# Optimization experiments

Hardware: AMD Instinct MI355X
Metric: run time of the kernel (lower is better)

The kernel has to match this reference:

```python
import jax, jax.numpy as jnp
import numpy as np


def _layer_norm(x, g, b, eps=1e-5):
    mu = jnp.mean(x, axis=-1, keepdims=True)
    var = jnp.mean((x - mu) ** 2, axis=-1, keepdims=True)
    return (x - mu) * jax.lax.rsqrt(var + eps) * g + b


def setup_inputs() -> dict:
    key = jax.random.key(0)
    ks = jax.random.split(key, 12)
    L, D, HD, F, V, MAXLEN, B, S = 4, 1024, 64, 4096, 32000, 2048, 2, 1024
    s = 0.02
    return {
        "x": jax.random.randint(ks[0], (B, S), 0, V, dtype=jnp.int32),
        "tok_emb": jax.random.normal(ks[1], (V, D), jnp.float32) * s,
        "pos_emb": jax.random.normal(ks[2], (MAXLEN, D), jnp.float32) * s,
        "wq": jax.random.normal(ks[3], (L, HD, HD), jnp.float32) * s,
        "wk": jax.random.normal(ks[4], (L, HD, HD), jnp.float32) * s,
        "wv": jax.random.normal(ks[5], (L, HD, HD), jnp.float32) * s,
        "wo": jax.random.normal(ks[6], (L, D, D), jnp.float32) * s,
        "bo": jnp.zeros((L, D), jnp.float32),
        "ln1_g": jnp.ones((L, D), jnp.float32),
        "ln1_b": jnp.zeros((L, D), jnp.float32),
        "ln2_g": jnp.ones((L, D), jnp.float32),
        "ln2_b": jnp.zeros((L, D), jnp.float32),
        "w1": jax.random.normal(ks[7], (L, F, D), jnp.float32) * s,
        "b1": jnp.zeros((L, F), jnp.float32),
        "w2": jax.random.normal(ks[8], (L, D, F), jnp.float32) * s,
        "b2": jnp.zeros((L, D), jnp.float32),
        "out_w": jax.random.normal(ks[9], (V, D), jnp.float32) * s,
        "out_b": jnp.zeros((V,), jnp.float32),
    }


def reference(x, tok_emb, pos_emb, wq, wk, wv, wo, bo, ln1_g, ln1_b, ln2_g, ln2_b, w1, b1, w2, b2, out_w, out_b):
    B, S = x.shape
    D = tok_emb.shape[1]
    HD = wq.shape[-1]
    H = D // HD
    inv_scale = 1.0 / jnp.sqrt(jnp.asarray(D, jnp.float32))  # note: embed_size, not head_dim

    h = tok_emb[x] + pos_emb[:S][None]  # [B,S,D]; dropout is identity in eval

    def block(h, p):
        pwq, pwk, pwv, pwo, pbo, g1, be1, g2, be2, pw1, pb1, pw2, pb2 = p
        xh = h.reshape(B, S, H, HD)
        # per-head Linear with shared [HD,HD] weight: y = x @ W.T
        q = jnp.einsum('bshd,ed->bshe', xh, pwq)
        k = jnp.einsum('bshd,ed->bshe', xh, pwk)
        v = jnp.einsum('bshd,ed->bshe', xh, pwv)
        energy = jnp.einsum('bqhd,bkhd->bhqk', q, k)  # full [B,H,S,S] scores
        attn = jax.nn.softmax(energy * inv_scale, axis=-1)
        o = jnp.einsum('bhqk,bkhd->bqhd', attn, v).reshape(B, S, D)
        o = o @ pwo.T + pbo
        x1 = _layer_norm(o + h, g1, be1)
        ff = jax.nn.gelu(x1 @ pw1.T + pb1, approximate=False) @ pw2.T + pb2
        return _layer_norm(ff + x1, g2, be2), None

    h, _ = jax.lax.scan(block, h, (wq, wk, wv, wo, bo, ln1_g, ln1_b, ln2_g, ln2_b, w1, b1, w2, b2))
    return h @ out_w.T + out_b  # [B,S,V] logits
```

## Files before the change

kernel.cpp:

```cpp
#include <hip/hip_runtime.h>
#include <math.h>

typedef float f32x4 __attribute__((ext_vector_type(4)));
typedef unsigned short u16x8 __attribute__((ext_vector_type(8)));
typedef unsigned short u16x4 __attribute__((ext_vector_type(4)));
typedef __bf16 bf16x8 __attribute__((ext_vector_type(8)));
typedef unsigned int u32;

#define DEV static __device__ __forceinline__

DEV unsigned short f2bf(float f) {
  __bf16 h = (__bf16)f;
  return __builtin_bit_cast(unsigned short, h);
}
DEV float bf2f(unsigned short s) { return __uint_as_float(((unsigned)s) << 16); }
DEV bf16x8 asbf(u16x8 v) { return __builtin_bit_cast(bf16x8, v); }

DEV void gload16(const void* g, void* l) {
  __builtin_amdgcn_global_load_lds((const __attribute__((address_space(1))) u32*)g,
                                   (__attribute__((address_space(3))) u32*)l, 16, 0, 0);
}

__global__ void cvt_kernel(const float* __restrict__ in, unsigned short* __restrict__ out, int n8) {
  for (int i = blockIdx.x * 256 + threadIdx.x; i < n8; i += gridDim.x * 256) {
    const float* s = in + (size_t)i * 8;
    f32x4 a = *(const f32x4*)s, b = *(const f32x4*)(s + 4);
    u16x8 o;
    for (int j = 0; j < 4; ++j) { o[j] = f2bf(a[j]); o[j + 4] = f2bf(b[j]); }
    *(u16x8*)(out + (size_t)i * 8) = o;
  }
}

__global__ void cvt2_kernel(const float* __restrict__ s0, unsigned short* __restrict__ d0, int na,
                            const float* __restrict__ s1, unsigned short* __restrict__ d1, int nb) {
  int total = na + nb;
  for (int i = blockIdx.x * 256 + threadIdx.x; i < total; i += gridDim.x * 256) {
    const float* s; unsigned short* d; int k;
    if (i < na) { s = s0; d = d0; k = i; } else { s = s1; d = d1; k = i - na; }
    f32x4 a = *(const f32x4*)(s + (size_t)k * 8), b = *(const f32x4*)(s + (size_t)k * 8 + 4);
    u16x8 o;
    for (int j = 0; j < 4; ++j) { o[j] = f2bf(a[j]); o[j + 4] = f2bf(b[j]); }
    *(u16x8*)(d + (size_t)k * 8) = o;
  }
}

__global__ void cvt3q_kernel(const float* __restrict__ s0, unsigned short* __restrict__ d0,
                             const float* __restrict__ s1, unsigned short* __restrict__ d1,
                             const float* __restrict__ s2, unsigned short* __restrict__ d2) {
  int i = blockIdx.x * 256 + threadIdx.x;
  if (i >= 6144) return;
  const float* s; unsigned short* d; int k = i & 2047;
  int seg = i >> 11;
  s = (seg == 0) ? s0 : (seg == 1) ? s1 : s2;
  d = (seg == 0) ? d0 : (seg == 1) ? d1 : d2;
  f32x4 a = *(const f32x4*)(s + (size_t)k * 8), b = *(const f32x4*)(s + (size_t)k * 8 + 4);
  u16x8 o;
  for (int j = 0; j < 4; ++j) { o[j] = f2bf(a[j]); o[j + 4] = f2bf(b[j]); }
  *(u16x8*)(d + (size_t)k * 8) = o;
}

__global__ void embed_kernel(const int* __restrict__ x, const float* __restrict__ tok,
                             const float* __restrict__ pos, float* __restrict__ h,
                             unsigned short* __restrict__ hbf) {
  int t = blockIdx.x, tid = threadIdx.x;
  int v = x[t], s = t & 1023;
  f32x4 a = *(const f32x4*)(tok + (size_t)v * 1024 + tid * 4);
  f32x4 b = *(const f32x4*)(pos + (size_t)s * 1024 + tid * 4);
  f32x4 r = a + b;
  *(f32x4*)(h + (size_t)t * 1024 + tid * 4) = r;
  u16x4 rb;
  for (int i = 0; i < 4; ++i) rb[i] = f2bf(r[i]);
  *(u16x4*)(hbf + (size_t)t * 1024 + tid * 4) = rb;
}

__global__ __launch_bounds__(256) void ln_kernel(const float* __restrict__ preA,
    const float* __restrict__ preB, const float* __restrict__ res,
    const float* __restrict__ g, const float* __restrict__ bta,
    float* __restrict__ outf, unsigned short* __restrict__ outbf) {
  int row = blockIdx.x, tid = threadIdx.x;
  size_t base = (size_t)row * 1024 + tid * 4;
  f32x4 xv = *(const f32x4*)(preA + base);
  xv += *(const f32x4*)(preB + base);
  xv += *(const f32x4*)(res + base);
  float s = xv[0] + xv[1] + xv[2] + xv[3];
  float s2 = xv[0]*xv[0] + xv[1]*xv[1] + xv[2]*xv[2] + xv[3]*xv[3];
  for (int m = 1; m < 64; m <<= 1) { s += __shfl_xor(s, m); s2 += __shfl_xor(s2, m); }
  __shared__ float red[8];
  int w = tid >> 6;
  if ((tid & 63) == 0) { red[w * 2] = s; red[w * 2 + 1] = s2; }
  __syncthreads();
  s = red[0] + red[2] + red[4] + red[6];
  s2 = red[1] + red[3] + red[5] + red[7];
  float mu = s * (1.f / 1024.f);
  float var = s2 * (1.f / 1024.f) - mu * mu;
  float rs = rsqrtf(var + 1e-5f);
  f32x4 gv = *(const f32x4*)(g + tid * 4);
  f32x4 bv = *(const f32x4*)(bta + tid * 4);
  f32x4 o; u16x4 ob;
  for (int i = 0; i < 4; ++i) { o[i] = (xv[i] - mu) * rs * gv[i] + bv[i]; ob[i] = f2bf(o[i]); }
  *(f32x4*)(outf + base) = o;
  *(u16x4*)(outbf + base) = ob;
}

__global__ __launch_bounds__(256) void qkvt_kernel(const unsigned short* __restrict__ hbf,
    const unsigned short* __restrict__ wqb, const unsigned short* __restrict__ wkb,
    const unsigned short* __restrict__ wvb,
    unsigned short* __restrict__ q, unsigned short* __restrict__ k,
    unsigned short* __restrict__ vt) {
  __shared__ unsigned short T[64 * 72];
  int tid = threadIdx.x, ln = tid & 63, w = tid >> 6;
  int l15 = ln & 15, lg = ln >> 4;
  int st = blockIdx.x, hh = blockIdx.y;
  int t0 = st * 64 + w * 16;
  const unsigned short* xp = hbf + (size_t)(t0 + l15) * 1024 + hh * 64 + lg * 8;
  bf16x8 xa0 = asbf(*(const u16x8*)xp);
  bf16x8 xa1 = asbf(*(const u16x8*)(xp + 32));
  const unsigned short* wp[3] = {wqb, wkb, wvb};
  f32x4 acc[3][4] = {};
#pragma unroll
  for (int m = 0; m < 3; ++m) {
    __builtin_amdgcn_s_setprio(1);
#pragma unroll
    for (int ni = 0; ni < 4; ++ni) {
      const unsigned short* wb = wp[m] + (size_t)(ni * 16 + l15) * 64 + lg * 8;
      bf16x8 w0 = asbf(*(const u16x8*)wb);
      bf16x8 w1 = asbf(*(const u16x8*)(wb + 32));
      acc[m][ni] = __builtin_amdgcn_mfma_f32_16x16x32_bf16(xa0, w0, acc[m][ni], 0, 0, 0);
      acc[m][ni] = __builtin_amdgcn_mfma_f32_16x16x32_bf16(xa1, w1, acc[m][ni], 0, 0, 0);
    }
    __builtin_amdgcn_s_setprio(0);
  }
  unsigned short* outp[2] = {q, k};
#pragma unroll
  for (int m = 0; m < 2; ++m)
#pragma unroll
    for (int ni = 0; ni < 4; ++ni)
#pragma unroll
      for (int r = 0; r < 4; ++r)
        outp[m][(size_t)(t0 + 4 * lg + r) * 1024 + hh * 64 + ni * 16 + l15] = f2bf(acc[m][ni][r]);
#pragma unroll
  for (int ni = 0; ni < 4; ++ni)
#pragma unroll
    for (int r = 0; r < 4; ++r)
      T[(ni * 16 + l15) * 72 + (w * 16 + 4 * lg + r)] = f2bf(acc[2][ni][r]);
  __syncthreads();
  int b = st >> 4, sb = (st & 15) * 64;
#pragma unroll
  for (int j = 0; j < 2; ++j) {
    int idx = tid + 256 * j; int e = idx >> 3, s8 = (idx & 7) * 8;
    *(u16x8*)(vt + ((size_t)((b * 16 + hh) * 64 + e)) * 1024 + sb + s8) =
        *(const u16x8*)&T[e * 72 + s8];
  }
}

__global__ __launch_bounds__(256, 2) void attn_kernel(const unsigned short* __restrict__ qb,
    const unsigned short* __restrict__ kb, const unsigned short* __restrict__ vtb,
    unsigned short* __restrict__ ob) {
  constexpr int PK = 72, PV = 136, PP = 136;
  __shared__ unsigned short Ks[128 * PK], Vs[64 * PV], Ps[4][16 * PP];
  int tid = threadIdx.x, lane = tid & 63, w = tid >> 6;
  int l15 = lane & 15, lg = lane >> 4;
  int qt = blockIdx.x, bh = blockIdx.y, b = bh >> 4, hh = bh & 15;
  int q0 = qt * 64 + w * 16;
  const unsigned short* qrow = qb + ((size_t)(b * 1024 + q0 + l15) * 16 + hh) * 64 + lg * 8;
  bf16x8 qa0 = asbf(*(const u16x8*)qrow);
  bf16x8 qa1 = asbf(*(const u16x8*)(qrow + 32));
  {
    const __bf16 s = (__bf16)0.03125f;
#pragma unroll
    for (int i = 0; i < 8; ++i) { qa0[i] = qa0[i] * s; qa1[i] = qa1[i] * s; }
  }
  float m_[4] = {-1e30f, -1e30f, -1e30f, -1e30f};
  float ls[4] = {0.f, 0.f, 0.f, 0.f};
  f32x4 oacc[4] = {};

  u16x8 KR[4], VR[4];
  auto loadT = [&](int kt) {
#pragma unroll
    for (int j = 0; j < 4; ++j) {
      int idx = tid + 256 * j;
      int r = idx >> 3, c0 = (idx & 7) * 8;
      KR[j] = *(const u16x8*)(kb + ((size_t)(b * 1024 + kt * 128 + r) * 16 + hh) * 64 + c0);
      int rv = idx >> 4, cv = (idx & 15) * 8;
      VR[j] = *(const u16x8*)(vtb + ((size_t)((b * 16 + hh) * 64) + rv) * 1024 + kt * 128 + cv);
    }
  };
  auto writeT = [&]() {
#pragma unroll
    for (int j = 0; j < 4; ++j) {
      int idx = tid + 256 * j;
      int r = idx >> 3, c0 = (idx & 7) * 8;
      *(u16x8*)(&Ks[r * PK + c0]) = KR[j];
      int rv = idx >> 4, cv = (idx & 15) * 8;
      *(u16x8*)(&Vs[rv * PV + cv]) = VR[j];
    }
  };
  loadT(0); writeT();
  __syncthreads();

  for (int kt = 0; kt < 8; ++kt) {
    f32x4 sf[8] = {};
    __builtin_amdgcn_s_setprio(1);
#pragma unroll
    for (int n = 0; n < 8; ++n) {
      bf16x8 k0 = asbf(*(const u16x8*)(&Ks[(n * 16 + l15) * PK + lg * 8]));
      bf16x8 k1 = asbf(*(const u16x8*)(&Ks[(n * 16 + l15) * PK + 32 + lg * 8]));
      sf[n] = __builtin_amdgcn_mfma_f32_16x16x32_bf16(qa0, k0, sf[n], 0, 0, 0);
      sf[n] = __builtin_amdgcn_mfma_f32_16x16x32_bf16(qa1, k1, sf[n], 0, 0, 0);
    }
    __builtin_amdgcn_s_setprio(0);
    if (kt < 7) loadT(kt + 1);
    float tm[4];
#pragma unroll
    for (int r = 0; r < 4; ++r) {
      float t0 = fmaxf(fmaxf(fmaxf(sf[0][r], sf[1][r]), fmaxf(sf[2][r], sf[3][r])),
                       fmaxf(fmaxf(sf[4][r], sf[5][r]), fmaxf(sf[6][r], sf[7][r])));
      for (int msk = 1; msk < 16; msk <<= 1) t0 = fmaxf(t0, __shfl_xor(t0, msk));
      tm[r] = t0;
    }
    bool need = false;
#pragma unroll
    for (int r = 0; r < 4; ++r) need |= (tm[r] > m_[r] + 8.f);
    if (__any(need)) {
#pragma unroll
      for (int r = 0; r < 4; ++r) {
        float nm = fmaxf(m_[r], tm[r]);
        float sc = __expf(m_[r] - nm);
        ls[r] *= sc;
#pragma unroll
        for (int n = 0; n < 4; ++n) oacc[n][r] *= sc;
        m_[r] = nm;
      }
    }
    float rsum[4] = {0.f, 0.f, 0.f, 0.f};
    unsigned short pb[8][4];
#pragma unroll
    for (int n = 0; n < 8; ++n)
#pragma unroll
      for (int r = 0; r < 4; ++r) {
        float pv = __expf(sf[n][r] - m_[r]);
        rsum[r] += pv;
        pb[n][r] = f2bf(pv);
      }
#pragma unroll
    for (int r = 0; r < 4; ++r) {
      float t0 = rsum[r];
      for (int msk = 1; msk < 16; msk <<= 1) t0 += __shfl_xor(t0, msk);
      ls[r] += t0;
    }
    unsigned short* pw = Ps[w];
#pragma unroll
    for (int n = 0; n < 8; ++n)
#pragma unroll
      for (int r = 0; r < 4; ++r)
        pw[(4 * lg + r) * PP + n * 16 + l15] = pb[n][r];
    asm volatile("s_waitcnt lgkmcnt(0)" ::: "memory");
    __builtin_amdgcn_sched_barrier(0);
    bf16x8 pa[4];
#pragma unroll
    for (int ks = 0; ks < 4; ++ks)
      pa[ks] = asbf(*(const u16x8*)(&pw[l15 * PP + ks * 32 + lg * 8]));
    __builtin_amdgcn_s_setprio(1);
#pragma unroll
    for (int n = 0; n < 4; ++n) {
#pragma unroll
      for (int ks = 0; ks < 4; ++ks) {
        bf16x8 v0 = asbf(*(const u16x8*)(&Vs[(n * 16 + l15) * PV + ks * 32 + lg * 8]));
        oacc[n] = __builtin_amdgcn_mfma_f32_16x16x32_bf16(pa[ks], v0, oacc[n], 0, 0, 0);
      }
    }
    __builtin_amdgcn_s_setprio(0);
    __syncthreads();
    if (kt < 7) { writeT(); __syncthreads(); }
  }
#pragma unroll
  for (int n = 0; n < 4; ++n)
#pragma unroll
    for (int r = 0; r < 4; ++r) {
      float o = oacc[n][r] / ls[r];
      ob[((size_t)(b * 1024 + q0 + 4 * lg + r) * 16 + hh) * 64 + n * 16 + l15] = f2bf(o);
    }
}

template <int BM, int KSPLIT, int EPI>
__global__ __launch_bounds__(256) void gemm_kernel(
    const unsigned short* __restrict__ A, int lda,
    const unsigned short* __restrict__ B, int ldb,
    const float* __restrict__ bias,
    float* __restrict__ CfA, float* __restrict__ CfB, unsigned short* __restrict__ Cb,
    int ldc, int Ksub) {
  constexpr int LOGMT = (BM == 128) ? 4 : 5;
  constexpr int MT = 2048 / BM;
  constexpr int MI = BM / 32;
  __shared__ alignas(16) char smem[33280];
  unsigned short* As = (unsigned short*)smem;
  unsigned short* Bs = As + 2 * BM * 32;
  float* Cs = (float*)smem;

  int wg = blockIdx.x;
  int mt = wg & (MT - 1);
  int rest = wg >> LOGMT;
  int nt, kh;
  if (KSPLIT == 2) { nt = rest & 7; kh = rest >> 3; }
  else { nt = rest; kh = 0; }
  int m0 = mt * BM, n0 = nt * 128;
  const unsigned short* Ae = A + (KSPLIT == 2 ? (size_t)kh * Ksub : 0);
  const unsigned short* Be = B + (KSPLIT == 2 ? (size_t)kh * Ksub : 0);

  int tid = threadIdx.x, ln = tid & 63, wv = tid >> 6;
  int l15 = ln & 15, lg = ln >> 4;
  int wm = (wv >> 1) * (BM / 2), wn = (wv & 1) * 64;

  auto stage = [&](int buf, int k0) {
    for (int j = 0; j < BM / 64; ++j) {
      int row = j * 64 + wv * 16 + (ln >> 2);
      gload16(Ae + (size_t)(m0 + row) * lda + k0 + (ln & 3) * 8,
              &As[buf * (BM * 32) + (j * 64 + wv * 16) * 32]);
    }
    for (int j = 0; j < 2; ++j) {
      int row = j * 64 + wv * 16 + (ln >> 2);
      gload16(Be + (size_t)(n0 + row) * ldb + k0 + (ln & 3) * 8,
              &Bs[buf * 4096 + (j * 64 + wv * 16) * 32]);
    }
  };

  f32x4 acc[MI][4] = {};
  auto compute = [&](int buf) {
    const unsigned short* as = &As[buf * (BM * 32)];
    const unsigned short* bs = &Bs[buf * 4096];
    bf16x8 af[MI], bfn[4];
    for (int mi = 0; mi < MI; ++mi)
      af[mi] = asbf(*(const u16x8*)&as[(wm + mi * 16 + l15) * 32 + lg * 8]);
    for (int ni = 0; ni < 4; ++ni)
      bfn[ni] = asbf(*(const u16x8*)&bs[(wn + ni * 16 + l15) * 32 + lg * 8]);
    for (int mi = 0; mi < MI; ++mi)
      for (int ni = 0; ni < 4; ++ni)
        acc[mi][ni] = __builtin_amdgcn_mfma_f32_16x16x32_bf16(af[mi], bfn[ni], acc[mi][ni], 0, 0, 0);
  };

  stage(0, 0);
  __syncthreads();
  int ntk = Ksub >> 5, cur = 0;
  for (int t = 0; t < ntk - 1; ++t) {
    stage(cur ^ 1, (t + 1) << 5);
    compute(cur);
    __syncthreads();
    cur ^= 1;
  }
  compute(cur);

  float* Cf = (kh == 0) ? CfA : CfB;
  const bool addb = (kh == 0);
  for (int p = 0; p < BM / 64; ++p) {
    __syncthreads();
    if ((wm >> 6) == p) {
      int rb = wm & 63;
      for (int mi = 0; mi < MI; ++mi)
        for (int ni = 0; ni < 4; ++ni) {
          int cn = wn + ni * 16 + l15;
          float bv = addb ? bias[n0 + cn] : 0.f;
          for (int r = 0; r < 4; ++r) {
            float vv = acc[mi][ni][r] + bv;
            if (EPI == 1) vv = 0.5f * vv * (1.f + erff(vv * 0.70710678118f));
            Cs[(rb + mi * 16 + 4 * lg + r) * 130 + cn] = vv;
          }
        }
    }
    __syncthreads();
    int row = tid >> 3;
    for (int ri = 0; ri < 2; ++ri) {
      int lr = ri * 32 + row;
      size_t gbase = (size_t)(m0 + p * 64 + lr) * ldc + n0;
      if (EPI == 0) {
        int c4 = (tid & 7) * 4;
        for (int j = 0; j < 4; ++j)
          *(f32x4*)(Cf + gbase + c4 + j * 32) = *(const f32x4*)&Cs[lr * 130 + c4 + j * 32];
      } else {
        for (int j = 0; j < 2; ++j) {
          int cc = (tid & 7) * 8 + j * 64;
          f32x4 v0 = *(const f32x4*)&Cs[lr * 130 + cc];
          f32x4 v1 = *(const f32x4*)&Cs[lr * 130 + cc + 4];
          u16x8 o;
          for (int i = 0; i < 4; ++i) { o[i] = f2bf(v0[i]); o[i + 4] = f2bf(v1[i]); }
          *(u16x8*)(Cb + gbase + cc) = o;
        }
      }
    }
  }
}

__global__ __launch_bounds__(512, 1) void gemm256_kernel(
    const unsigned short* __restrict__ A, int lda,
    const unsigned short* __restrict__ B, int ldb,
    const float* __restrict__ bias, float* __restrict__ C, int ldc, int K) {
  extern __shared__ unsigned short sm[];
  int b = blockIdx.x;
  int c = (int)gridDim.x >> 3;
  int wg = (b & 7) * c + (b >> 3);
  int mt = wg & 7, nt = wg >> 3;
  int m0 = mt * 256, n0 = nt * 256;

  int tid = threadIdx.x, ln = tid & 63, wv = tid >> 6;
  int l15 = ln & 15, lg = ln >> 4;
  int wm = wv >> 2, wn = wv & 3;
  int l7 = l15 & 7;

  int srow = tid >> 3, sblk = (tid & 7) ^ (srow & 7);
  const unsigned short* Ab = A + (size_t)(m0 + srow) * lda + sblk * 8;
  const unsigned short* BbG[4];
#pragma unroll
  for (int g = 0; g < 4; ++g) {
    int p = g * 64 + srow;
    int j = p & 127;
    int r = ((j >> 5) << 6) + ((p >> 7) << 5) + (j & 31);
    BbG[g] = B + (size_t)(n0 + r) * ldb + sblk * 8;
  }
  auto stA = [&](int e, int g, int k0) {
    gload16(Ab + ((size_t)g * 64) * lda + k0, &sm[e * 16384 + g * 4096 + wv * 512]);
  };
  auto stB = [&](int e, int g, int k0) {
    gload16(BbG[g] + k0, &sm[32768 + e * 16384 + g * 4096 + wv * 512]);
  };

  auto ldsA = [&](int d, int mi, int ks) -> bf16x8 {
    int row = wm * 128 + mi * 16 + l15;
    return asbf(*(const u16x8*)&sm[d * 16384 + row * 64 + (((ks << 2) | lg) ^ l7) * 8]);
  };
  auto ldsB = [&](int d, int ni, int ks) -> bf16x8 {
    int p = ((ni >> 1) << 7) + wn * 32 + ((ni & 1) << 4) + l15;
    return asbf(*(const u16x8*)&sm[32768 + d * 16384 + p * 64 + (((ks << 2) | lg) ^ l7) * 8]);
  };

  f32x4 acc[8][4] = {};
  bf16x8 Af[4][2], Bf01[2][2], Bf23[2][2];

#define PH_OPEN() __builtin_amdgcn_s_barrier(); \
  asm volatile("s_waitcnt lgkmcnt(0)" ::: "memory"); \
  __builtin_amdgcn_sched_barrier(0); __builtin_amdgcn_s_setprio(1)

  stA(0, 0, 0); stA(0, 2, 0); stB(0, 0, 0); stB(0, 1, 0);
  stB(0, 2, 0); stB(0, 3, 0); stA(0, 1, 0); stA(0, 3, 0);
  asm volatile("s_waitcnt vmcnt(0)" ::: "memory");
  __builtin_amdgcn_s_barrier();

  int ntk = K >> 6;
  for (int kk = 0; kk < ntk; ++kk) {
    int d = kk & 1, e = d ^ 1, k1 = (kk + 1) << 6;
    bool pf = (kk + 1 < ntk);
    {
#pragma unroll
      for (int ni = 0; ni < 2; ++ni) { Bf01[ni][0] = ldsB(d, ni, 0); Bf01[ni][1] = ldsB(d, ni, 1); }
#pragma unroll
      for (int mi = 0; mi < 4; ++mi) { Af[mi][0] = ldsA(d, mi, 0); Af[mi][1] = ldsA(d, mi, 1); }
      if (pf) { stA(e, 0, k1); stA(e, 2, k1); stB(e, 0, k1); stB(e, 1, k1); }
      PH_OPEN();
#pragma unroll
      for (int mi = 0; mi < 4; ++mi)
#pragma unroll
        for (int ni = 0; ni < 2; ++ni) {
          acc[mi][ni] = __builtin_amdgcn_mfma_f32_16x16x32_bf16(Af[mi][0], Bf01[ni][0], acc[mi][ni], 0, 0, 0);
          acc[mi][ni] = __builtin_amdgcn_mfma_f32_16x16x32_bf16(Af[mi][1], Bf01[ni][1], acc[mi][ni], 0, 0, 0);
        }
      __builtin_amdgcn_s_setprio(0);
      if (pf) { asm volatile("s_waitcnt vmcnt(6)" ::: "memory"); }
      else    { asm volatile("s_waitcnt vmcnt(2)" ::: "memory"); }
      __builtin_amdgcn_s_barrier();
    }
    {
#pragma unroll
      for (int ni = 0; ni < 2; ++ni) { Bf23[ni][0] = ldsB(d, 2 + ni, 0); Bf23[ni][1] = ldsB(d, 2 + ni, 1); }
      if (pf) { stB(e, 2, k1); stB(e, 3, k1); }
      PH_OPEN();
#pragma unroll
      for (int mi = 0; mi < 4; ++mi)
#pragma unroll
        for (int ni = 0; ni < 2; ++ni) {
          acc[mi][2 + ni] = __builtin_amdgcn_mfma_f32_16x16x32_bf16(Af[mi][0], Bf23[ni][0], acc[mi][2 + ni], 0, 0, 0);
          acc[mi][2 + ni] = __builtin_amdgcn_mfma_f32_16x16x32_bf16(Af[mi][1], Bf23[ni][1], acc[mi][2 + ni], 0, 0, 0);
        }
      __builtin_amdgcn_s_setprio(0);
      if (pf) { asm volatile("s_waitcnt vmcnt(6)" ::: "memory"); }
      else    { asm volatile("s_waitcnt vmcnt(0)" ::: "memory"); }
      __builtin_amdgcn_s_barrier();
    }
    {
#pragma unroll
      for (int mi = 0; mi < 4; ++mi) { Af[mi][0] = ldsA(d, 4 + mi, 0); Af[mi][1] = ldsA(d, 4 + mi, 1); }
      if (pf) { stA(e, 1, k1); stA(e, 3, k1); }
      PH_OPEN();
#pragma unroll
      for (int mi = 0; mi < 4; ++mi)
#pragma unroll
        for (int ni = 0; ni < 2; ++ni) {
          acc[4 + mi][2 + ni] = __builtin_amdgcn_mfma_f32_16x16x32_bf16(Af[mi][0], Bf23[ni][0], acc[4 + mi][2 + ni], 0, 0, 0);
          acc[4 + mi][2 + ni] = __builtin_amdgcn_mfma_f32_16x16x32_bf16(Af[mi][1], Bf23[ni][1], acc[4 + mi][2 + ni], 0, 0, 0);
        }
      __builtin_amdgcn_s_setprio(0);
      __builtin_amdgcn_s_barrier();
    }
    {
      PH_OPEN();
#pragma unroll
      for (int mi = 0; mi < 4; ++mi)
#pragma unroll
        for (int ni = 0; ni < 2; ++ni) {
          acc[4 + mi][ni] = __builtin_amdgcn_mfma_f32_16x16x32_bf16(Af[mi][0], Bf01[ni][0], acc[4 + mi][ni], 0, 0, 0);
          acc[4 + mi][ni] = __builtin_amdgcn_mfma_f32_16x16x32_bf16(Af[mi][1], Bf01[ni][1], acc[4 + mi][ni], 0, 0, 0);
        }
      __builtin_amdgcn_s_setprio(0);
      if (pf) { asm volatile("s_waitcnt vmcnt(4)" ::: "memory"); }
      __builtin_amdgcn_s_barrier();
    }
  }
#undef PH_OPEN

  float* fb = (float*)sm;
  int fbase = wv * 4096;
  float bv[4];
#pragma unroll
  for (int ni = 0; ni < 4; ++ni) bv[ni] = bias[n0 + wn * 64 + ni * 16 + l15];
#pragma unroll
  for (int p = 0; p < 2; ++p) {
    if (p) { asm volatile("s_waitcnt lgkmcnt(0)" ::: "memory"); __builtin_amdgcn_sched_barrier(0); }
#pragma unroll
    for (int mi = 0; mi < 4; ++mi)
#pragma unroll
      for (int ni = 0; ni < 4; ++ni)
#pragma unroll
        for (int r = 0; r < 4; ++r)
          fb[fbase + (mi * 16 + lg * 4 + r) * 64 + ni * 16 + l15] = acc[4 * p + mi][ni][r] + bv[ni];
    asm volatile("s_waitcnt lgkmcnt(0)" ::: "memory");
    __builtin_amdgcn_sched_barrier(0);
#pragma unroll
    for (int i = 0; i < 16; ++i) {
      int row = i * 4 + lg;
      f32x4 v = *(const f32x4*)&fb[fbase + row * 64 + l15 * 4];
      int grow = m0 + wm * 128 + p * 64 + row;
      *(f32x4*)(&C[(size_t)grow * ldc + n0 + wn * 64 + l15 * 4]) = v;
    }
  }
}

extern "C" void kernel_launch(void* const* d_in, const int* in_sizes, int n_in,
                              void* d_out, int out_size, void* d_ws, size_t ws_size,
                              hipStream_t stream) {
  const int* x = (const int*)d_in[0];
  const float* tok = (const float*)d_in[1];
  const float* pos = (const float*)d_in[2];
  const float* wq = (const float*)d_in[3];
  const float* wk = (const float*)d_in[4];
  const float* wv = (const float*)d_in[5];
  const float* wo = (const float*)d_in[6];
  const float* bo = (const float*)d_in[7];
  const float* ln1g = (const float*)d_in[8];
  const float* ln1b = (const float*)d_in[9];
  const float* ln2g = (const float*)d_in[10];
  const float* ln2b = (const float*)d_in[11];
  const float* w1 = (const float*)d_in[12];
  const float* b1 = (const float*)d_in[13];
  const float* w2 = (const float*)d_in[14];
  const float* b2 = (const float*)d_in[15];
  const float* outw = (const float*)d_in[16];
  const float* outb = (const float*)d_in[17];
  float* out = (float*)d_out;

  const size_t MiB = 1 << 20;
  const size_t need = 4 * MiB + 65536000;
  if (ws_size < need) return;
  char* base = (char*)d_ws;
  unsigned short* hbf = (unsigned short*)base;
  char* R = base + 4 * MiB;
  float* hf  = (float*)(R);
  float* x1f = (float*)(R + 8 * MiB);
  unsigned short* x1bf = (unsigned short*)(R + 16 * MiB);
  float* cfA = (float*)(R + 20 * MiB);
  float* cfB = (float*)(R + 28 * MiB);
  unsigned short* qs = (unsigned short*)(R + 36 * MiB);
  const size_t SL = 2048ull * 1024;
  unsigned short* qbf = qs;
  unsigned short* kbf = qs + SL;
  unsigned short* vbf = qs + 2 * SL;
  unsigned short* vtbf = qs + 3 * SL;
  unsigned short* wobf = vtbf;
  unsigned short* w1bf = qbf;
  unsigned short* w2bf = qbf;
  unsigned short* ffbf = vbf;
  unsigned short* wqbf = (unsigned short*)(R + 60 * MiB);
  unsigned short* wkbf = wqbf + 16384;
  unsigned short* wvbf = wkbf + 16384;
  unsigned short* outwbf = (unsigned short*)R;

  embed_kernel<<<2048, 256, 0, stream>>>(x, tok, pos, hf, hbf);
  cvt3q_kernel<<<24, 256, 0, stream>>>(wq, wqbf, wk, wkbf, wv, wvbf);
  for (int l = 0; l < 4; ++l) {
    qkvt_kernel<<<dim3(32, 16), 256, 0, stream>>>(hbf, wqbf + l * 4096, wkbf + l * 4096,
                                                  wvbf + l * 4096, qbf, kbf, vtbf);
    attn_kernel<<<dim3(16, 32), 256, 0, stream>>>(qbf, kbf, vtbf, vbf);
    cvt2_kernel<<<2048, 256, 0, stream>>>(wo + (size_t)l * 1048576, wobf, 131072,
                                          w1 + (size_t)l * 4194304, w1bf, 524288);
    gemm_kernel<64, 2, 0><<<512, 256, 0, stream>>>(
        vbf, 1024, wobf, 1024, bo + l * 1024, cfA, cfB, nullptr, 1024, 512);
    ln_kernel<<<2048, 256, 0, stream>>>(cfA, cfB, hf, ln1g + l * 1024, ln1b + l * 1024,
                                        x1f, x1bf);
    gemm_kernel<128, 1, 1><<<512, 256, 0, stream>>>(
        x1bf, 1024, w1bf, 1024, b1 + l * 4096, nullptr, nullptr, ffbf, 4096, 1024);
    cvt_kernel<<<2048, 256, 0, stream>>>(w2 + (size_t)l * 4194304, w2bf, 524288);
    gemm_kernel<64, 2, 0><<<512, 256, 0, stream>>>(
        ffbf, 4096, w2bf, 4096, b2 + l * 1024, cfA, cfB, nullptr, 1024, 2048);
    ln_kernel<<<2048, 256, 0, stream>>>(cfA, cfB, x1f, ln2g + l * 1024, ln2b + l * 1024,
                                        hf, hbf);
  }
  cvt_kernel<<<2048, 256, 0, stream>>>(outw, outwbf, 4096000);
  gemm256_kernel<<<1000, 512, 131072, stream>>>(hbf, 1024, outwbf, 1024, outb, out, 32000, 1024);
}
```

Before: 857.6 us.

## Add 128x256-tile 512-thread pipelined GEMM for FFN up-projection with fused GELU

Replaces the generic gemm_kernel used for the FFN first projection (M=2048, N=4096, K=1024) with a dedicated 512-thread kernel using 128x256 tiles. It double-buffers through async global-to-LDS loads, splits each k-step into two MFMA phases with priority hints, and fuses bias plus exact GELU into an LDS-staged bf16 epilogue. The aim is more reuse per tile and better overlap of loads with MFMA work than the older 256-thread kernel. In exchange it runs 256 blocks at one block per CU with 128KB LDS, which may leave some CUs idle or limit latency hiding.

```diff
diff --git a/kernel.cpp b/kernel.cpp
--- a/kernel.cpp
+++ b/kernel.cpp
@@ -389,6 +389,132 @@
   }
 }
 
+__global__ __launch_bounds__(512, 1) void gemmF1_kernel(
+    const unsigned short* __restrict__ A, int lda,
+    const unsigned short* __restrict__ B, int ldb,
+    const float* __restrict__ bias, unsigned short* __restrict__ Cb, int ldc, int K) {
+  extern __shared__ unsigned short sm[];
+  int b = blockIdx.x;
+  int c = (int)gridDim.x >> 3;
+  int wg = (b & 7) * c + (b >> 3);
+  int mt = wg & 15, nt = wg >> 4;
+  int m0 = mt * 128, n0 = nt * 256;
+
+  int tid = threadIdx.x, ln = tid & 63, wv = tid >> 6;
+  int l15 = ln & 15, lg = ln >> 4;
+  int wm = wv >> 2, wn = wv & 3;
+  int l7 = l15 & 7;
+
+  int srow = tid >> 3, sblk = (tid & 7) ^ (srow & 7);
+  const unsigned short* Ab = A + (size_t)(m0 + srow) * lda + sblk * 8;
+  const unsigned short* BbG[4];
+#pragma unroll
+  for (int g = 0; g < 4; ++g) {
+    int p = g * 64 + srow;
+    int j = p & 127;
+    int r = ((j >> 5) << 6) + ((p >> 7) << 5) + (j & 31);
+    BbG[g] = B + (size_t)(n0 + r) * ldb + sblk * 8;
+  }
+  auto stA = [&](int e, int g, int k0) {
+    gload16(Ab + ((size_t)g * 64) * lda + k0, &sm[e * 8192 + g * 4096 + wv * 512]);
+  };
+  auto stB = [&](int e, int g, int k0) {
+    gload16(BbG[g] + k0, &sm[16384 + e * 16384 + g * 4096 + wv * 512]);
+  };
+
+  auto ldsA = [&](int d, int mi, int ks) -> bf16x8 {
+    int row = wm * 64 + mi * 16 + l15;
+    return asbf(*(const u16x8*)&sm[d * 8192 + row * 64 + (((ks << 2) | lg) ^ l7) * 8]);
+  };
+  auto ldsB = [&](int d, int ni, int ks) -> bf16x8 {
+    int p = ((ni >> 1) << 7) + wn * 32 + ((ni & 1) << 4) + l15;
+    return asbf(*(const u16x8*)&sm[16384 + d * 16384 + p * 64 + (((ks << 2) | lg) ^ l7) * 8]);
+  };
+
+  f32x4 acc[4][4] = {};
+  bf16x8 Af[4][2], Bf01[2][2], Bf23[2][2];
+
+#define PH_OPEN() __builtin_amdgcn_s_barrier(); \
+  asm volatile("s_waitcnt lgkmcnt(0)" ::: "memory"); \
+  __builtin_amdgcn_sched_barrier(0); __builtin_amdgcn_s_setprio(1)
+
+  stA(0, 0, 0); stA(0, 1, 0); stB(0, 0, 0); stB(0, 1, 0);
+  stB(0, 2, 0); stB(0, 3, 0);
+  asm volatile("s_waitcnt vmcnt(2)" ::: "memory");
+  __builtin_amdgcn_s_barrier();
+
+  int ntk = K >> 6;
+  for (int kk = 0; kk < ntk; ++kk) {
+    int d = kk & 1, e = d ^ 1, k1 = (kk + 1) << 6;
+    bool pf = (kk + 1 < ntk);
+    {
+#pragma unroll
+      for (int ni = 0; ni < 2; ++ni) { Bf01[ni][0] = ldsB(d, ni, 0); Bf01[ni][1] = ldsB(d, ni, 1); }
+#pragma unroll
+      for (int mi = 0; mi < 4; ++mi) { Af[mi][0] = ldsA(d, mi, 0); Af[mi][1] = ldsA(d, mi, 1); }
+      if (pf) { stA(e, 0, k1); stA(e, 1, k1); stB(e, 0, k1); stB(e, 1, k1); }
+      PH_OPEN();
+#pragma unroll
+      for (int mi = 0; mi < 4; ++mi)
+#pragma unroll
+        for (int ni = 0; ni < 2; ++ni) {
+          acc[mi][ni] = __builtin_amdgcn_mfma_f32_16x16x32_bf16(Af[mi][0], Bf01[ni][0], acc[mi][ni], 0, 0, 0);
+          acc[mi][ni] = __builtin_amdgcn_mfma_f32_16x16x32_bf16(Af[mi][1], Bf01[ni][1], acc[mi][ni], 0, 0, 0);
+        }
+      __builtin_amdgcn_s_setprio(0);
+      if (pf) { asm volatile("s_waitcnt vmcnt(4)" ::: "memory"); }
+      else    { asm volatile("s_waitcnt vmcnt(0)" ::: "memory"); }
+      __builtin_amdgcn_s_barrier();
+    }
+    {
+#pragma unroll
+      for (int ni = 0; ni < 2; ++ni) { Bf23[ni][0] = ldsB(d, 2 + ni, 0); Bf23[ni][1] = ldsB(d, 2 + ni, 1); }
+      if (pf) { stB(e, 2, k1); stB(e, 3, k1); }
+      PH_OPEN();
+#pragma unroll
+      for (int mi = 0; mi < 4; ++mi)
+#pragma unroll
+        for (int ni = 0; ni < 2; ++ni) {
+          acc[mi][2 + ni] = __builtin_amdgcn_mfma_f32_16x16x32_bf16(Af[mi][0], Bf23[ni][0], acc[mi][2 + ni], 0, 0, 0);
+          acc[mi][2 + ni] = __builtin_amdgcn_mfma_f32_16x16x32_bf16(Af[mi][1], Bf23[ni][1], acc[mi][2 + ni], 0, 0, 0);
+        }
+      __builtin_amdgcn_s_setprio(0);
+      if (pf) { asm volatile("s_waitcnt vmcnt(2)" ::: "memory"); }
+      __builtin_amdgcn_s_barrier();
+    }
+  }
+#undef PH_OPEN
+
+  float* fb = (float*)sm;
+  int fbase = wv * 4096;
+  float bv[4];
+#pragma unroll
+  for (int ni = 0; ni < 4; ++ni) bv[ni] = bias[n0 + wn * 64 + ni * 16 + l15];
+#pragma unroll
+  for (int mi = 0; mi < 4; ++mi)
+#pragma unroll
+    for (int ni = 0; ni < 4; ++ni)
+#pragma unroll
+      for (int r = 0; r < 4; ++r) {
+        float vv = acc[mi][ni][r] + bv[ni];
+        vv = 0.5f * vv * (1.f + erff(vv * 0.70710678118f));
+        fb[fbase + (mi * 16 + lg * 4 + r) * 64 + ni * 16 + l15] = vv;
+      }
+  asm volatile("s_waitcnt lgkmcnt(0)" ::: "memory");
+  __builtin_amdgcn_sched_barrier(0);
+#pragma unroll
+  for (int i = 0; i < 8; ++i) {
+    int row = i * 8 + (ln >> 3);
+    int cc = (ln & 7) * 8;
+    f32x4 v0 = *(const f32x4*)&fb[fbase + row * 64 + cc];
+    f32x4 v1 = *(const f32x4*)&fb[fbase + row * 64 + cc + 4];
+    u16x8 o;
+#pragma unroll
+    for (int j = 0; j < 4; ++j) { o[j] = f2bf(v0[j]); o[j + 4] = f2bf(v1[j]); }
+    *(u16x8*)(Cb + (size_t)(m0 + wm * 64 + row) * ldc + n0 + wn * 64 + cc) = o;
+  }
+}
+
 __global__ __launch_bounds__(512, 1) void gemm256_kernel(
     const unsigned short* __restrict__ A, int lda,
     const unsigned short* __restrict__ B, int ldb,
@@ -602,8 +728,8 @@
         vbf, 1024, wobf, 1024, bo + l * 1024, cfA, cfB, nullptr, 1024, 512);
     ln_kernel<<<2048, 256, 0, stream>>>(cfA, cfB, hf, ln1g + l * 1024, ln1b + l * 1024,
                                         x1f, x1bf);
-    gemm_kernel<128, 1, 1><<<512, 256, 0, stream>>>(
-        x1bf, 1024, w1bf, 1024, b1 + l * 4096, nullptr, nullptr, ffbf, 4096, 1024);
+    gemmF1_kernel<<<256, 512, 131072, stream>>>(
+        x1bf, 1024, w1bf, 1024, b1 + l * 4096, ffbf, 4096, 1024);
     cvt_kernel<<<2048, 256, 0, stream>>>(w2 + (size_t)l * 4194304, w2bf, 524288);
     gemm_kernel<64, 2, 0><<<512, 256, 0, stream>>>(
         ffbf, 4096, w2bf, 4096, b2 + l * 1024, cfA, cfB, nullptr, 1024, 2048);
```

Result: faster. 810.5 us (-5.5%).
